# Optimization experiments

Hardware: AMD Instinct MI355X
Metric: run time of the kernel (lower is better)

The kernel has to match this reference:

```python
import jax, jax.numpy as jnp
import numpy as np

B, C, H, W = 16, 512, 64, 64
L, D = 77, 768
NH = 8
HD = C // NH
EPS = 1e-5


def layernorm(x, g, b):
    m = jnp.mean(x, axis=-1, keepdims=True)
    v = jnp.var(x, axis=-1, keepdims=True)
    return (x - m) * jax.lax.rsqrt(v + EPS) * g + b


def setup_inputs() -> dict:
    key = jax.random.key(0)
    ks = jax.random.split(key, 12)
    s_c = 1.0 / np.sqrt(C)
    s_d = 1.0 / np.sqrt(D)
    return {
        "x": jax.random.normal(ks[0], (B, C, H, W), jnp.float32),
        "text_features": jax.random.normal(ks[1], (B, L, D), jnp.float32),
        "wq": jax.random.normal(ks[2], (C, C), jnp.float32) * s_c,
        "bq": jnp.zeros((C,), jnp.float32),
        "wk": jax.random.normal(ks[3], (C, D), jnp.float32) * s_d,
        "bk": jnp.zeros((C,), jnp.float32),
        "wv": jax.random.normal(ks[4], (C, D), jnp.float32) * s_d,
        "bv": jnp.zeros((C,), jnp.float32),
        "wo": jax.random.normal(ks[5], (C, C), jnp.float32) * s_c,
        "bo": jnp.zeros((C,), jnp.float32),
        "g1": jnp.ones((C,), jnp.float32),
        "b1": jnp.zeros((C,), jnp.float32),
        "g2": jnp.ones((C,), jnp.float32),
        "b2": jnp.zeros((C,), jnp.float32),
    }


def reference(x, text_features, wq, bq, wk, bk, wv, bv, wo, bo, g1, b1, g2, b2):
    b, c, h, w = x.shape
    # 1x1 conv query projection
    q = jnp.einsum('bchw,oc->bohw', x, wq) + bq[None, :, None, None]
    # 2D positional encoding: first c/2 channels vary along w, next c/2 along h
    pos_x = jnp.broadcast_to(jnp.linspace(0.0, 1.0, w)[None, :], (h, w))
    pos_y = jnp.broadcast_to(jnp.linspace(0.0, 1.0, h)[:, None], (h, w))
    pe = jnp.concatenate([
        jnp.broadcast_to(pos_x[None], (c // 2, h, w)),
        jnp.broadcast_to(pos_y[None], (c // 2, h, w)),
    ], axis=0)  # [C,H,W]
    q = q + 0.05 * pe[None]
    # flatten spatial -> tokens, layernorm over channels
    q_flat = q.reshape(b, c, h * w).transpose(0, 2, 1)  # [B,HW,C]
    q_norm = layernorm(q_flat, g1, b1)
    qh = q_norm.reshape(b, h * w, NH, HD)  # [B,HW,NH,HD]
    # text key/value projections
    k = jnp.einsum('bld,cd->blc', text_features, wk) + bk
    v = jnp.einsum('bld,cd->blc', text_features, wv) + bv
    k_norm = layernorm(k, g2, b2)
    kh = k_norm.reshape(b, -1, NH, HD)
    vh = v.reshape(b, -1, NH, HD)
    scale = HD ** -0.5
    attn = jnp.einsum('bqhd,bkhd->bhqk', qh, kh) * scale  # [B,NH,HW,L]
    attn = jax.nn.softmax(attn, axis=-1)  # dropout is identity in eval
    out = jnp.einsum('bhqk,bkhd->bqhd', attn, vh).reshape(b, h * w, c)
    out = out.transpose(0, 2, 1).reshape(b, c, h, w)
    out = jnp.einsum('bchw,oc->bohw', out, wo) + bo[None, :, None, None]
    return out + x
```

## Files before the change

### kernel.cpp

```cpp
#include <hip/hip_runtime.h>
#include <stdint.h>

#define BD   16
#define CD   512
#define HD_  64
#define NH_  8
#define HWD  4096
#define LD   77
#define DD   768

typedef __bf16 bf16;
typedef bf16 bf16x8 __attribute__((ext_vector_type(8)));
typedef float f32x4 __attribute__((ext_vector_type(4)));

__device__ __forceinline__ void async16(const bf16* g, bf16* l) {
  __builtin_amdgcn_global_load_lds(
      (const __attribute__((address_space(1))) void*)g,
      (__attribute__((address_space(3))) void*)l, 16, 0, 0);
}

__device__ __forceinline__ unsigned short bfb(float f) {
  bf16 h = (bf16)f;
  return __builtin_bit_cast(unsigned short, h);
}

__global__ __launch_bounds__(256) void xpose_cvt(const float* __restrict__ X,
                                                 bf16* __restrict__ Y) {
  __shared__ float tile[64][68];
  const int b = blockIdx.z, c0 = blockIdx.y * 64, t0 = blockIdx.x * 64;
  const int tid = threadIdx.x;
  const float* Xb = X + ((size_t)b * CD + c0) * HWD + t0;
#pragma unroll
  for (int p = 0; p < 4; ++p) {
    int c = (tid >> 4) + p * 16;
    int t = (tid & 15) * 4;
    float4 v = *(const float4*)(Xb + (size_t)c * HWD + t);
    *(float4*)&tile[c][t] = v;
  }
  __syncthreads();
  int t = tid >> 2, cb = (tid & 3) * 16;
  union { uint4 u[2]; unsigned short us[16]; } pk;
#pragma unroll
  for (int j = 0; j < 16; ++j) pk.us[j] = bfb(tile[cb + j][t]);
  uint4* Yp = (uint4*)(Y + ((size_t)(b * HWD + t0 + t)) * CD + c0 + cb);
  Yp[0] = pk.u[0];
  Yp[1] = pk.u[1];
}

__global__ void cvt_bf16_k(const float* __restrict__ X, bf16* __restrict__ Y, int n) {
  int i = (blockIdx.x * 256 + threadIdx.x) * 8;
  if (i >= n) return;
  float4 a = *(const float4*)(X + i);
  float4 c = *(const float4*)(X + i + 4);
  union { uint4 u; unsigned short us[8]; } pk;
  pk.us[0] = bfb(a.x); pk.us[1] = bfb(a.y); pk.us[2] = bfb(a.z); pk.us[3] = bfb(a.w);
  pk.us[4] = bfb(c.x); pk.us[5] = bfb(c.y); pk.us[6] = bfb(c.z); pk.us[7] = bfb(c.w);
  *(uint4*)(Y + i) = pk.u;
}

template <int TM, int TN, int MODE>
__global__ __launch_bounds__(256)
void gemm_bt(const bf16* __restrict__ A, const bf16* __restrict__ B,
             int M, int N, int K,
             const float* __restrict__ bias, const float* __restrict__ xres,
             float* __restrict__ D) {
  constexpr int WM = TM / 2, WN = TN / 2;
  constexpr int AFR = WM / 16, BFR = WN / 16;
  constexpr int ACH = TM / 8, TCH = (TM + TN) / 8, WCH = TCH / 4;
  __shared__ bf16 sA[TM * 64];
  __shared__ bf16 sB[TN * 64];
  const int tid = threadIdx.x, wave = tid >> 6, lane = tid & 63;
  const int m0 = blockIdx.y * TM, n0 = blockIdx.x * TN;
  const int wm = (wave >> 1) * WM, wn = (wave & 1) * WN;
  const int sub = lane >> 3, col8 = (lane & 7) * 8;
  const int mlo = lane & 15, khi = lane >> 4;
  f32x4 acc[AFR][BFR] = {};

  for (int k0 = 0; k0 < K; k0 += 64) {
#pragma unroll
    for (int r = 0; r < WCH; ++r) {
      int ci = wave * WCH + r;
      if (ci < ACH) {
        int row = ci * 8 + sub;
        int g = m0 + row;
        if (g > M - 1) g = M - 1;
        async16(A + (size_t)g * K + k0 + col8, &sA[ci * 512]);
      } else {
        int cj = ci - ACH;
        int row = cj * 8 + sub;
        async16(B + (size_t)(n0 + row) * K + k0 + col8, &sB[cj * 512]);
      }
    }
    __syncthreads();
#pragma unroll
    for (int kc = 0; kc < 2; ++kc) {
      bf16x8 af[AFR], bfv[BFR];
      const int ko = kc * 32 + khi * 8;
#pragma unroll
      for (int i = 0; i < AFR; ++i)
        af[i] = *(const bf16x8*)&sA[(wm + i * 16 + mlo) * 64 + ko];
#pragma unroll
      for (int j = 0; j < BFR; ++j)
        bfv[j] = *(const bf16x8*)&sB[(wn + j * 16 + mlo) * 64 + ko];
#pragma unroll
      for (int i = 0; i < AFR; ++i)
#pragma unroll
        for (int j = 0; j < BFR; ++j)
          acc[i][j] = __builtin_amdgcn_mfma_f32_16x16x32_bf16(af[i], bfv[j],
                                                              acc[i][j], 0, 0, 0);
    }
    __syncthreads();
  }

#pragma unroll
  for (int i = 0; i < AFR; ++i) {
    const int mb = m0 + wm + i * 16 + khi * 4;
#pragma unroll
    for (int j = 0; j < BFR; ++j) {
      const int n = n0 + wn + j * 16 + mlo;
#pragma unroll
      for (int r = 0; r < 4; ++r) {
        const int m = mb + r;
        float val = acc[i][j][r];
        if constexpr (MODE == 0) {
          int hw = m & (HWD - 1);
          float pe = (n < 256) ? (float)(hw & 63) : (float)(hw >> 6);
          val += bias[n] + (0.05f / 63.0f) * pe;
          D[(size_t)m * CD + n] = val;
        } else if constexpr (MODE == 1) {
          if (m < M) D[(size_t)m * CD + n] = val + bias[n];
        } else {
          int b = n >> 12, hw = n & (HWD - 1);
          size_t addr = ((size_t)(b * CD + m)) * HWD + hw;
          D[addr] = val + bias[m] + xres[addr];
        }
      }
    }
  }
}

__global__ __launch_bounds__(256) void ln_rows(const float* __restrict__ X,
                                               const float* __restrict__ gg,
                                               const float* __restrict__ bb,
                                               bf16* __restrict__ Y, int nrows,
                                               int khlayout) {
  const int wv = threadIdx.x >> 6, lane = threadIdx.x & 63;
  const int row = blockIdx.x * 4 + wv;
  if (row >= nrows) return;
  const float* xr = X + (size_t)row * CD + lane * 8;
  float4 v0 = *(const float4*)xr;
  float4 v1 = *(const float4*)(xr + 4);
  float xv[8] = {v0.x, v0.y, v0.z, v0.w, v1.x, v1.y, v1.z, v1.w};
  float s = 0.f, sq = 0.f;
#pragma unroll
  for (int j = 0; j < 8; ++j) { s += xv[j]; sq += xv[j] * xv[j]; }
#pragma unroll
  for (int off = 1; off < 64; off <<= 1) {
    s += __shfl_xor(s, off);
    sq += __shfl_xor(sq, off);
  }
  float mean = s * (1.0f / 512.0f);
  float var = sq * (1.0f / 512.0f) - mean * mean;
  float rstd = rsqrtf(var + 1e-5f);
  const int c0 = lane * 8;
  union { uint4 u; unsigned short us[8]; } pk;
#pragma unroll
  for (int j = 0; j < 8; ++j)
    pk.us[j] = bfb((xv[j] - mean) * rstd * gg[c0 + j] + bb[c0 + j]);
  size_t ya;
  if (khlayout) {
    int bq = row / LD, l = row - bq * LD;
    int hh = lane >> 3, dd = (lane & 7) * 8;
    ya = (((size_t)(bq * NH_ + hh)) * LD + l) * HD_ + dd;
  } else {
    ya = (size_t)row * CD + c0;
  }
  *(uint4*)(Y + ya) = pk.u;
}

__global__ __launch_bounds__(256) void make_vt(const float* __restrict__ vraw,
                                               bf16* __restrict__ vt) {
  const int bh = blockIdx.x, b = bh >> 3, h = bh & 7;
  const int tid = threadIdx.x, d = tid & 63, lg = tid >> 6;
  for (int l = lg; l < 96; l += 4) {
    float v = 0.f;
    if (l < LD) v = vraw[((size_t)(b * LD + l)) * CD + h * HD_ + d];
    vt[((size_t)(bh * HD_ + d)) * 96 + l] = (bf16)v;
  }
}

__global__ __launch_bounds__(256) void attn_k(const bf16* __restrict__ Q,
                                              const bf16* __restrict__ KH,
                                              const bf16* __restrict__ VT,
                                              bf16* __restrict__ O) {
  __shared__ bf16 P[4][16 * 104];
  const int tid = threadIdx.x, wv = tid >> 6, lane = tid & 63;
  const int m = lane & 15, kg = lane >> 4;
  const int q0 = blockIdx.x * 64, h = blockIdx.y, b = blockIdx.z;
  const int bh = b * NH_ + h;

  const size_t qoff = ((size_t)(b * HWD + q0 + wv * 16 + m)) * CD + h * HD_;
  bf16x8 a0 = *(const bf16x8*)(Q + qoff + kg * 8);
  bf16x8 a1 = *(const bf16x8*)(Q + qoff + 32 + kg * 8);

  const bf16* Kb = KH + (size_t)bh * LD * HD_;
  f32x4 s[5];
#pragma unroll
  for (int kt = 0; kt < 5; ++kt) {
    int key = kt * 16 + m;
    if (key > LD - 1) key = LD - 1;
    const bf16* kr = Kb + key * HD_ + kg * 8;
    bf16x8 b0 = *(const bf16x8*)kr;
    bf16x8 b1 = *(const bf16x8*)(kr + 32);
    f32x4 z = {0.f, 0.f, 0.f, 0.f};
    z = __builtin_amdgcn_mfma_f32_16x16x32_bf16(a0, b0, z, 0, 0, 0);
    z = __builtin_amdgcn_mfma_f32_16x16x32_bf16(a1, b1, z, 0, 0, 0);
    s[kt] = z;
  }

  bf16* Pw = &P[wv][0];
#pragma unroll
  for (int r = 0; r < 4; ++r) {
    float sc[5];
#pragma unroll
    for (int kt = 0; kt < 5; ++kt) {
      float v = s[kt][r] * 0.125f;
      if (kt == 4 && m >= LD - 64) v = -3.0e38f;
      sc[kt] = v;
    }
    float mx = fmaxf(fmaxf(fmaxf(sc[0], sc[1]), fmaxf(sc[2], sc[3])), sc[4]);
    mx = fmaxf(mx, __shfl_xor(mx, 1));
    mx = fmaxf(mx, __shfl_xor(mx, 2));
    mx = fmaxf(mx, __shfl_xor(mx, 4));
    mx = fmaxf(mx, __shfl_xor(mx, 8));
    float sum = 0.f;
#pragma unroll
    for (int kt = 0; kt < 5; ++kt) {
      sc[kt] = __expf(sc[kt] - mx);
      sum += sc[kt];
    }
    sum += __shfl_xor(sum, 1);
    sum += __shfl_xor(sum, 2);
    sum += __shfl_xor(sum, 4);
    sum += __shfl_xor(sum, 8);
    float inv = 1.0f / sum;
    const int prow = kg * 4 + r;
#pragma unroll
    for (int kt = 0; kt < 5; ++kt)
      Pw[prow * 104 + kt * 16 + m] = (bf16)(sc[kt] * inv);
    Pw[prow * 104 + 80 + m] = (bf16)0.f;
  }
  __syncthreads();

  bf16x8 ap[3];
#pragma unroll
  for (int kc = 0; kc < 3; ++kc)
    ap[kc] = *(const bf16x8*)&Pw[m * 104 + kc * 32 + kg * 8];

  const bf16* Vb = VT + (size_t)bh * HD_ * 96;
  f32x4 o[4] = {};
#pragma unroll
  for (int nt = 0; nt < 4; ++nt) {
#pragma unroll
    for (int kc = 0; kc < 3; ++kc) {
      bf16x8 bv = *(const bf16x8*)(Vb + (nt * 16 + m) * 96 + kc * 32 + kg * 8);
      o[nt] = __builtin_amdgcn_mfma_f32_16x16x32_bf16(ap[kc], bv, o[nt], 0, 0, 0);
    }
  }
#pragma unroll
  for (int nt = 0; nt < 4; ++nt)
#pragma unroll
    for (int r = 0; r < 4; ++r) {
      const int row = b * HWD + q0 + wv * 16 + kg * 4 + r;
      O[(size_t)row * CD + h * HD_ + nt * 16 + m] = (bf16)(o[nt][r]);
    }
}

extern "C" void kernel_launch(void* const* d_in, const int* in_sizes, int n_in,
                              void* d_out, int out_size, void* d_ws, size_t ws_size,
                              hipStream_t stream) {
  const float* x    = (const float*)d_in[0];
  const float* text = (const float*)d_in[1];
  const float* wq   = (const float*)d_in[2];
  const float* bq   = (const float*)d_in[3];
  const float* wk   = (const float*)d_in[4];
  const float* bk   = (const float*)d_in[5];
  const float* wv   = (const float*)d_in[6];
  const float* bv   = (const float*)d_in[7];
  const float* wo   = (const float*)d_in[8];
  const float* bo   = (const float*)d_in[9];
  const float* g1   = (const float*)d_in[10];
  const float* b1   = (const float*)d_in[11];
  const float* g2   = (const float*)d_in[12];
  const float* b2   = (const float*)d_in[13];
  float* out = (float*)d_out;

  char* p = (char*)d_ws;
  auto alloc = [&](size_t bytes) {
    char* r = p;
    p += (bytes + 255) & ~(size_t)255;
    return r;
  };
  bf16* xt     = (bf16*)alloc((size_t)BD * HWD * CD * 2);
  bf16* attn_o = (bf16*)alloc((size_t)BD * HWD * CD * 2);
  bf16* textb  = (bf16*)alloc((size_t)BD * LD * DD * 2);
  bf16* wqb    = (bf16*)alloc((size_t)CD * CD * 2);
  bf16* wkb    = (bf16*)alloc((size_t)CD * DD * 2);
  bf16* wvb    = (bf16*)alloc((size_t)CD * DD * 2);
  bf16* wob    = (bf16*)alloc((size_t)CD * CD * 2);
  float* kraw  = (float*)alloc((size_t)BD * LD * CD * 4);
  float* vraw  = (float*)alloc((size_t)BD * LD * CD * 4);
  bf16* kh     = (bf16*)alloc((size_t)BD * NH_ * LD * HD_ * 2);
  bf16* vt     = (bf16*)alloc((size_t)BD * NH_ * HD_ * 96 * 2);
  float* qraw = out;
  bf16* qbf = xt;

  xpose_cvt<<<dim3(HWD / 64, CD / 64, BD), 256, 0, stream>>>(x, xt);
  const int nt_ = BD * LD * DD;
  cvt_bf16_k<<<(nt_ / 8 + 255) / 256, 256, 0, stream>>>(text, textb, nt_);
  cvt_bf16_k<<<(CD * CD / 8 + 255) / 256, 256, 0, stream>>>(wq, wqb, CD * CD);
  cvt_bf16_k<<<(CD * DD / 8 + 255) / 256, 256, 0, stream>>>(wk, wkb, CD * DD);
  cvt_bf16_k<<<(CD * DD / 8 + 255) / 256, 256, 0, stream>>>(wv, wvb, CD * DD);
  cvt_bf16_k<<<(CD * CD / 8 + 255) / 256, 256, 0, stream>>>(wo, wob, CD * CD);

  gemm_bt<128, 128, 1><<<dim3(4, 10), 256, 0, stream>>>(
      textb, wkb, BD * LD, CD, DD, bk, nullptr, kraw);
  gemm_bt<128, 128, 1><<<dim3(4, 10), 256, 0, stream>>>(
      textb, wvb, BD * LD, CD, DD, bv, nullptr, vraw);
  ln_rows<<<(BD * LD) / 4, 256, 0, stream>>>(kraw, g2, b2, kh, BD * LD, 1);
  make_vt<<<BD * NH_, 256, 0, stream>>>(vraw, vt);

  gemm_bt<128, 256, 0><<<dim3(2, 512), 256, 0, stream>>>(
      xt, wqb, BD * HWD, CD, CD, bq, nullptr, qraw);
  ln_rows<<<(BD * HWD) / 4, 256, 0, stream>>>(qraw, g1, b1, qbf, BD * HWD, 0);

  attn_k<<<dim3(HWD / 64, NH_, BD), 256, 0, stream>>>(qbf, kh, vt, attn_o);

  gemm_bt<256, 128, 3><<<dim3(512, 2), 256, 0, stream>>>(
      wob, attn_o, CD, BD * HWD, CD, bo, x, out);
}
```

Baseline: 627.6 us.

## Fuse query GEMM with bias, positional encoding and LayerNorm; retile output GEMM

The query projection kernel now has each block compute a full 64x512 row tile, so bias, positional encoding and the channel LayerNorm are applied in the epilogue. It writes bf16 normalized queries directly, removing the fp32 intermediate and the separate LayerNorm pass. The output projection is restructured similarly with full-M tiles per block. Weights in both kernels are read straight from global memory rather than LDS, which depends on cache reuse and may raise load latency.

```diff
diff --git a/kernel.cpp b/kernel.cpp
--- a/kernel.cpp
+++ b/kernel.cpp
@@ -58,15 +58,12 @@
   *(uint4*)(Y + i) = pk.u;
 }
 
-template <int TM, int TN, int MODE>
 __global__ __launch_bounds__(256)
-void gemm_bt(const bf16* __restrict__ A, const bf16* __restrict__ B,
-             int M, int N, int K,
-             const float* __restrict__ bias, const float* __restrict__ xres,
+void gemm_kv(const bf16* __restrict__ A, const bf16* __restrict__ B,
+             int M, int K, const float* __restrict__ bias,
              float* __restrict__ D) {
-  constexpr int WM = TM / 2, WN = TN / 2;
-  constexpr int AFR = WM / 16, BFR = WN / 16;
-  constexpr int ACH = TM / 8, TCH = (TM + TN) / 8, WCH = TCH / 4;
+  constexpr int TM = 128, TN = 128;
+  constexpr int WM = 64, WN = 64, AFR = 4, BFR = 4;
   __shared__ bf16 sA[TM * 64];
   __shared__ bf16 sB[TN * 64];
   const int tid = threadIdx.x, wave = tid >> 6, lane = tid & 63;
@@ -78,15 +75,15 @@
 
   for (int k0 = 0; k0 < K; k0 += 64) {
 #pragma unroll
-    for (int r = 0; r < WCH; ++r) {
-      int ci = wave * WCH + r;
-      if (ci < ACH) {
+    for (int r = 0; r < 8; ++r) {
+      int ci = wave * 8 + r;
+      if (ci < 16) {
         int row = ci * 8 + sub;
         int g = m0 + row;
         if (g > M - 1) g = M - 1;
         async16(A + (size_t)g * K + k0 + col8, &sA[ci * 512]);
       } else {
-        int cj = ci - ACH;
+        int cj = ci - 16;
         int row = cj * 8 + sub;
         async16(B + (size_t)(n0 + row) * K + k0 + col8, &sB[cj * 512]);
       }
@@ -121,29 +118,164 @@
 #pragma unroll
       for (int r = 0; r < 4; ++r) {
         const int m = mb + r;
-        float val = acc[i][j][r];
-        if constexpr (MODE == 0) {
-          int hw = m & (HWD - 1);
-          float pe = (n < 256) ? (float)(hw & 63) : (float)(hw >> 6);
-          val += bias[n] + (0.05f / 63.0f) * pe;
-          D[(size_t)m * CD + n] = val;
-        } else if constexpr (MODE == 1) {
-          if (m < M) D[(size_t)m * CD + n] = val + bias[n];
-        } else {
-          int b = n >> 12, hw = n & (HWD - 1);
-          size_t addr = ((size_t)(b * CD + m)) * HWD + hw;
-          D[addr] = val + bias[m] + xres[addr];
-        }
-      }
-    }
-  }
-}
-
-__global__ __launch_bounds__(256) void ln_rows(const float* __restrict__ X,
-                                               const float* __restrict__ gg,
-                                               const float* __restrict__ bb,
-                                               bf16* __restrict__ Y, int nrows,
-                                               int khlayout) {
+        if (m < M) D[(size_t)m * CD + n] = acc[i][j][r] + bias[n];
+      }
+    }
+  }
+}
+
+__global__ __launch_bounds__(256)
+void gemm_q_ln(const bf16* __restrict__ A, const bf16* __restrict__ B,
+               const float* __restrict__ bq, const float* __restrict__ g1,
+               const float* __restrict__ b1, bf16* __restrict__ Y) {
+  __shared__ bf16 sA[64 * 64];
+  __shared__ float sStat[64][8];
+  const int tid = threadIdx.x, wave = tid >> 6, lane = tid & 63;
+  const int m0 = blockIdx.x * 64;
+  const int wn = wave * 128;
+  const int mlo = lane & 15, khi = lane >> 4;
+  const int sub = lane >> 3, col8 = (lane & 7) * 8;
+  f32x4 acc[4][8] = {};
+
+  for (int k0 = 0; k0 < CD; k0 += 64) {
+    async16(A + (size_t)(m0 + wave * 8 + sub) * CD + k0 + col8,
+            &sA[wave * 8 * 64]);
+    async16(A + (size_t)(m0 + 32 + wave * 8 + sub) * CD + k0 + col8,
+            &sA[(32 + wave * 8) * 64]);
+    __syncthreads();
+#pragma unroll
+    for (int kc = 0; kc < 2; ++kc) {
+      const int ko = kc * 32 + khi * 8;
+      bf16x8 af[4];
+#pragma unroll
+      for (int i = 0; i < 4; ++i)
+        af[i] = *(const bf16x8*)&sA[(i * 16 + mlo) * 64 + ko];
+      const bf16* Bp = B + (size_t)(wn + mlo) * CD + k0 + ko;
+#pragma unroll
+      for (int j = 0; j < 8; ++j) {
+        bf16x8 bv = *(const bf16x8*)(Bp + (size_t)j * 16 * CD);
+#pragma unroll
+        for (int i = 0; i < 4; ++i)
+          acc[i][j] = __builtin_amdgcn_mfma_f32_16x16x32_bf16(af[i], bv,
+                                                              acc[i][j], 0, 0, 0);
+      }
+    }
+    __syncthreads();
+  }
+
+  float bqf[8], g1f[8], b1f[8];
+#pragma unroll
+  for (int j = 0; j < 8; ++j) {
+    int col = wn + j * 16 + mlo;
+    bqf[j] = bq[col];
+    g1f[j] = g1[col];
+    b1f[j] = b1[col];
+  }
+  const float pescale = 0.05f / 63.0f;
+#pragma unroll
+  for (int i = 0; i < 4; ++i) {
+#pragma unroll
+    for (int r = 0; r < 4; ++r) {
+      int rloc = i * 16 + khi * 4 + r;
+      int hw = (m0 + rloc) & (HWD - 1);
+      float pe = (float)((wn < 256) ? (hw & 63) : (hw >> 6)) * pescale;
+      float s = 0.f, sq = 0.f;
+#pragma unroll
+      for (int j = 0; j < 8; ++j) {
+        float v = acc[i][j][r] + bqf[j] + pe;
+        acc[i][j][r] = v;
+        s += v;
+        sq += v * v;
+      }
+#pragma unroll
+      for (int off = 1; off < 16; off <<= 1) {
+        s += __shfl_xor(s, off);
+        sq += __shfl_xor(sq, off);
+      }
+      if (mlo == 0) {
+        sStat[rloc][wave * 2] = s;
+        sStat[rloc][wave * 2 + 1] = sq;
+      }
+    }
+  }
+  __syncthreads();
+#pragma unroll
+  for (int i = 0; i < 4; ++i) {
+#pragma unroll
+    for (int r = 0; r < 4; ++r) {
+      int rloc = i * 16 + khi * 4 + r;
+      float s = sStat[rloc][0] + sStat[rloc][2] + sStat[rloc][4] + sStat[rloc][6];
+      float sq = sStat[rloc][1] + sStat[rloc][3] + sStat[rloc][5] + sStat[rloc][7];
+      float mean = s * (1.0f / 512.0f);
+      float var = sq * (1.0f / 512.0f) - mean * mean;
+      float rstd = rsqrtf(var + 1e-5f);
+      bf16* yr = Y + (size_t)(m0 + rloc) * CD + wn + mlo;
+#pragma unroll
+      for (int j = 0; j < 8; ++j)
+        yr[j * 16] = (bf16)((acc[i][j][r] - mean) * rstd * g1f[j] + b1f[j]);
+    }
+  }
+}
+
+__global__ __launch_bounds__(256)
+void gemm_o(const bf16* __restrict__ Wo, const bf16* __restrict__ AO,
+            const float* __restrict__ bo, const float* __restrict__ xres,
+            float* __restrict__ out) {
+  __shared__ bf16 sB[64 * 64];
+  const int tid = threadIdx.x, wave = tid >> 6, lane = tid & 63;
+  const int n0 = blockIdx.x * 64;
+  const int wm = wave * 128;
+  const int mlo = lane & 15, khi = lane >> 4;
+  const int sub = lane >> 3, col8 = (lane & 7) * 8;
+  f32x4 acc[8][4] = {};
+
+  for (int k0 = 0; k0 < CD; k0 += 64) {
+    async16(AO + (size_t)(n0 + wave * 8 + sub) * CD + k0 + col8,
+            &sB[wave * 8 * 64]);
+    async16(AO + (size_t)(n0 + 32 + wave * 8 + sub) * CD + k0 + col8,
+            &sB[(32 + wave * 8) * 64]);
+    __syncthreads();
+#pragma unroll
+    for (int kc = 0; kc < 2; ++kc) {
+      const int ko = kc * 32 + khi * 8;
+      bf16x8 bfv[4];
+#pragma unroll
+      for (int j = 0; j < 4; ++j)
+        bfv[j] = *(const bf16x8*)&sB[(j * 16 + mlo) * 64 + ko];
+      const bf16* Ap = Wo + (size_t)(wm + mlo) * CD + k0 + ko;
+#pragma unroll
+      for (int i = 0; i < 8; ++i) {
+        bf16x8 av = *(const bf16x8*)(Ap + (size_t)i * 16 * CD);
+#pragma unroll
+        for (int j = 0; j < 4; ++j)
+          acc[i][j] = __builtin_amdgcn_mfma_f32_16x16x32_bf16(av, bfv[j],
+                                                              acc[i][j], 0, 0, 0);
+      }
+    }
+    __syncthreads();
+  }
+
+#pragma unroll
+  for (int i = 0; i < 8; ++i) {
+#pragma unroll
+    for (int r = 0; r < 4; ++r) {
+      const int m = wm + i * 16 + khi * 4 + r;
+      const float bom = bo[m];
+#pragma unroll
+      for (int j = 0; j < 4; ++j) {
+        const int n = n0 + j * 16 + mlo;
+        const int b = n >> 12, hw = n & (HWD - 1);
+        size_t addr = ((size_t)(b * CD + m)) * HWD + hw;
+        out[addr] = acc[i][j][r] + bom + xres[addr];
+      }
+    }
+  }
+}
+
+__global__ __launch_bounds__(256) void ln_rows_k(const float* __restrict__ X,
+                                                 const float* __restrict__ gg,
+                                                 const float* __restrict__ bb,
+                                                 bf16* __restrict__ Y, int nrows) {
   const int wv = threadIdx.x >> 6, lane = threadIdx.x & 63;
   const int row = blockIdx.x * 4 + wv;
   if (row >= nrows) return;
@@ -167,14 +299,9 @@
 #pragma unroll
   for (int j = 0; j < 8; ++j)
     pk.us[j] = bfb((xv[j] - mean) * rstd * gg[c0 + j] + bb[c0 + j]);
-  size_t ya;
-  if (khlayout) {
-    int bq = row / LD, l = row - bq * LD;
-    int hh = lane >> 3, dd = (lane & 7) * 8;
-    ya = (((size_t)(bq * NH_ + hh)) * LD + l) * HD_ + dd;
-  } else {
-    ya = (size_t)row * CD + c0;
-  }
+  int bq = row / LD, l = row - bq * LD;
+  int hh = lane >> 3, dd = (lane & 7) * 8;
+  size_t ya = (((size_t)(bq * NH_ + hh)) * LD + l) * HD_ + dd;
   *(uint4*)(Y + ya) = pk.u;
 }
 
@@ -312,7 +439,6 @@
   float* vraw  = (float*)alloc((size_t)BD * LD * CD * 4);
   bf16* kh     = (bf16*)alloc((size_t)BD * NH_ * LD * HD_ * 2);
   bf16* vt     = (bf16*)alloc((size_t)BD * NH_ * HD_ * 96 * 2);
-  float* qraw = out;
   bf16* qbf = xt;
 
   xpose_cvt<<<dim3(HWD / 64, CD / 64, BD), 256, 0, stream>>>(x, xt);
@@ -323,19 +449,14 @@
   cvt_bf16_k<<<(CD * DD / 8 + 255) / 256, 256, 0, stream>>>(wv, wvb, CD * DD);
   cvt_bf16_k<<<(CD * CD / 8 + 255) / 256, 256, 0, stream>>>(wo, wob, CD * CD);
 
-  gemm_bt<128, 128, 1><<<dim3(4, 10), 256, 0, stream>>>(
-      textb, wkb, BD * LD, CD, DD, bk, nullptr, kraw);
-  gemm_bt<128, 128, 1><<<dim3(4, 10), 256, 0, stream>>>(
-      textb, wvb, BD * LD, CD, DD, bv, nullptr, vraw);
-  ln_rows<<<(BD * LD) / 4, 256, 0, stream>>>(kraw, g2, b2, kh, BD * LD, 1);
+  gemm_kv<<<dim3(4, 10), 256, 0, stream>>>(textb, wkb, BD * LD, DD, bk, kraw);
+  gemm_kv<<<dim3(4, 10), 256, 0, stream>>>(textb, wvb, BD * LD, DD, bv, vraw);
+  ln_rows_k<<<(BD * LD + 3) / 4, 256, 0, stream>>>(kraw, g2, b2, kh, BD * LD);
   make_vt<<<BD * NH_, 256, 0, stream>>>(vraw, vt);
 
-  gemm_bt<128, 256, 0><<<dim3(2, 512), 256, 0, stream>>>(
-      xt, wqb, BD * HWD, CD, CD, bq, nullptr, qraw);
-  ln_rows<<<(BD * HWD) / 4, 256, 0, stream>>>(qraw, g1, b1, qbf, BD * HWD, 0);
+  gemm_q_ln<<<dim3(BD * HWD / 64), 256, 0, stream>>>(xt, wqb, bq, g1, b1, qbf);
 
   attn_k<<<dim3(HWD / 64, NH_, BD), 256, 0, stream>>>(qbf, kh, vt, attn_o);
 
-  gemm_bt<256, 128, 3><<<dim3(512, 2), 256, 0, stream>>>(
-      wob, attn_o, CD, BD * HWD, CD, bo, x, out);
-}
+  gemm_o<<<dim3(BD * HWD / 64), 256, 0, stream>>>(wob, attn_o, bo, x, out);
+}
```

Measured after the change: 669.4 us. 1.07x slower.
